# Performance work log

Measured on AMD Instinct MI355X. Metric: run time of the kernel, lower is better.

Reference implementation:

```python
import jax, jax.numpy as jnp
from jax import lax
import numpy as np

NPOINT = 1024
NSAMPLE = 32
BN_EPS = 1e-3  # Keras BatchNormalization default epsilon


def farthest_point_sample(xyz, npoint):
    # xyz: [B, N, 3] -> indices [B, npoint] (int32), sequential O(npoint*N)
    B, N, _ = xyz.shape

    def step(carry, _):
        distance, farthest = carry                                   # [B,N], [B]
        centroid = jnp.take_along_axis(xyz, farthest[:, None, None], axis=1)  # [B,1,3]
        dist = jnp.sum((xyz - centroid) ** 2, axis=-1)               # [B,N]
        distance = jnp.minimum(distance, dist)
        new_farthest = jnp.argmax(distance, axis=1).astype(jnp.int32)
        return (distance, new_farthest), farthest

    init = (jnp.full((B, N), 1e10, xyz.dtype), jnp.zeros((B,), jnp.int32))
    _, idxs = lax.scan(step, init, xs=None, length=npoint)           # [npoint, B]
    return jnp.transpose(idxs)                                       # [B, npoint]


def index_points_2d(points, idx):
    # points: [B,N,C], idx: [B,S] -> [B,S,C]
    return jnp.take_along_axis(points, idx[:, :, None], axis=1)


def index_points_3d(points, idx):
    # points: [B,N,C], idx: [B,S,K] -> [B,S,K,C]
    return jax.vmap(lambda p, i: p[i])(points, idx)


def query_ball_point(nsample, xyz, new_xyz):
    # nearest-nsample variant (radius is ignored, matching the source)
    # sq_dist: [B, S, N]
    sq = jnp.sum(new_xyz ** 2, axis=-1, keepdims=True) \
         - 2.0 * jnp.einsum('bsc,bnc->bsn', new_xyz, xyz) \
         + jnp.sum(xyz ** 2, axis=-1)[:, None, :]
    _, group_idx = lax.top_k(-sq, nsample)                           # [B,S,K]
    return group_idx


def bn_relu(x, g, b, mm, mv):
    # inference-mode BatchNorm (moving stats) + ReLU, per-channel on last dim
    return jax.nn.relu((x - mm) * lax.rsqrt(mv + BN_EPS) * g + b)


def setup_inputs() -> dict:
    key = jax.random.key(0)
    ks = jax.random.split(key, 20)
    B, N, D = 4, 16384, 64
    mlp = [64, 64, 128]
    cin = 3 + D  # 67
    inp = {
        'xyz': jax.random.normal(ks[0], (B, N, 3), jnp.float32),
        'points': jax.random.normal(ks[1], (B, N, D), jnp.float32),
    }
    c = cin
    for i, co in enumerate(mlp):
        inp[f'w{i}'] = jax.random.normal(ks[2 + 4 * i], (c, co), jnp.float32) * (1.0 / np.sqrt(c))
        inp[f'g{i}'] = jnp.ones((co,), jnp.float32)
        inp[f'b{i}'] = jnp.zeros((co,), jnp.float32)
        inp[f'mm{i}'] = jax.random.normal(ks[3 + 4 * i], (co,), jnp.float32) * 0.1
        inp[f'mv{i}'] = jax.random.uniform(ks[4 + 4 * i], (co,), jnp.float32, 0.5, 1.5)
        c = co
    return inp


def reference(xyz, points, w0, g0, b0, mm0, mv0, w1, g1, b1, mm1, mv1, w2, g2, b2, mm2, mv2):
    fps_idx = farthest_point_sample(xyz, NPOINT)                     # [B,S]
    new_xyz = index_points_2d(xyz, fps_idx)                          # [B,S,3]
    idx = query_ball_point(NSAMPLE, xyz, new_xyz)                    # [B,S,K]
    grouped_xyz = index_points_3d(xyz, idx)                          # [B,S,K,3]
    grouped_xyz_norm = grouped_xyz - new_xyz[:, :, None, :]
    grouped_points = index_points_3d(points, idx)                    # [B,S,K,D]
    x = jnp.concatenate([grouped_xyz_norm, grouped_points], axis=-1) # [B,S,K,3+D]
    for w, g, b, mm, mv in ((w0, g0, b0, mm0, mv0), (w1, g1, b1, mm1, mv1), (w2, g2, b2, mm2, mv2)):
        x = bn_relu(jnp.einsum('bskc,co->bsko', x, w), g, b, mm, mv)
    new_points = jnp.max(x, axis=2)                                  # [B,S,C_out]
    return (new_xyz, new_points)
```

## Files before the change

### kernel.cpp

```cpp
#include <hip/hip_runtime.h>
#include <hip/hip_bf16.h>
#include <stdint.h>

#define N_PTS 16384
#define S_OUT 1024


__global__ __launch_bounds__(1024) void fps_kernel(
    const float* __restrict__ xyz,
    float* __restrict__ out_newxyz)
{
  const int b    = blockIdx.x;
  const int tid  = threadIdx.x;
  const int lane = tid & 63;
  const int wid  = tid >> 6;
  const float* base = xyz + (size_t)b * N_PTS * 3;

  float px[16], py[16], pz[16], dist[16];
#pragma unroll
  for (int i = 0; i < 16; ++i) {
    int n = tid * 16 + i;
    px[i] = base[n * 3 + 0];
    py[i] = base[n * 3 + 1];
    pz[i] = base[n * 3 + 2];
    dist[i] = 1e10f;
  }

  __shared__ unsigned long long sred[2][16];

  float cx = base[0], cy = base[1], cz = base[2];

  for (int s = 0; s < S_OUT; ++s) {
    if (tid == 0) {
      size_t o = ((size_t)b * S_OUT + s) * 3;
      out_newxyz[o + 0] = cx;
      out_newxyz[o + 1] = cy;
      out_newxyz[o + 2] = cz;
    }
    if (s == S_OUT - 1) break;

    float best  = -1.0f;
    int   bestI = 0;
#pragma unroll
    for (int i = 0; i < 16; ++i) {
      float dx = __fsub_rn(px[i], cx);
      float dy = __fsub_rn(py[i], cy);
      float dz = __fsub_rn(pz[i], cz);
      float dd = __fadd_rn(__fadd_rn(__fmul_rn(dx, dx), __fmul_rn(dy, dy)),
                           __fmul_rn(dz, dz));
      float dm = fminf(dist[i], dd);
      dist[i] = dm;
      bool c = dm > best;
      best  = c ? dm : best;
      bestI = c ? i  : bestI;
    }
    const unsigned bestN = (unsigned)(tid * 16 + bestI);

    float m = best;
#pragma unroll
    for (int off = 1; off < 64; off <<= 1)
      m = fmaxf(m, __shfl_xor(m, off));
    unsigned long long msk = __ballot(best == m);
    int wl = __ffsll(msk) - 1;
    unsigned wn = (unsigned)__shfl((int)bestN, wl);

    const int p = s & 1;
    if (lane == 0)
      sred[p][wid] = ((unsigned long long)__float_as_uint(m) << 32) |
                     (unsigned long long)(0xFFFFFFFFu - wn);
    __syncthreads();

    unsigned long long k = sred[p][lane & 15];
#pragma unroll
    for (int off = 1; off < 16; off <<= 1) {
      unsigned long long o = __shfl_xor(k, off);
      if (o > k) k = o;
    }
    unsigned n = 0xFFFFFFFFu - (unsigned)(k & 0xFFFFFFFFull);
    n = __builtin_amdgcn_readfirstlane(n);
    const float* pc = base + (size_t)n * 3;
    cx = pc[0]; cy = pc[1]; cz = pc[2];
  }
}

__global__ __launch_bounds__(256, 2) void knn_kernel(
    const float* __restrict__ xyz,
    const float* __restrict__ newxyz,
    int* __restrict__ knn_out)
{
  const int bs  = blockIdx.x;
  const int b   = bs >> 10;
  const int tid = threadIdx.x;
  const float* base = xyz + (size_t)b * N_PTS * 3;

  const float qx = newxyz[(size_t)bs * 3 + 0];
  const float qy = newxyz[(size_t)bs * 3 + 1];
  const float qz = newxyz[(size_t)bs * 3 + 2];
  const float sumq = __fadd_rn(__fadd_rn(__fmul_rn(qx, qx), __fmul_rn(qy, qy)),
                               __fmul_rn(qz, qz));

  __shared__ unsigned hist[2048];
  __shared__ unsigned tsum[256];
  __shared__ unsigned long long cand[512];
  __shared__ unsigned long long s_min;
  __shared__ int s_b1, s_r1, s_b2, s_r2, s_cntL, s_cntC;

  for (int i = tid; i < 2048; i += 256) hist[i] = 0;
  if (tid == 0) { s_cntL = 0; s_cntC = 0; }
  __syncthreads();

#define KNN_KEY(n, u)                                                          \
    float x = base[(n) * 3 + 0];                                               \
    float y = base[(n) * 3 + 1];                                               \
    float z = base[(n) * 3 + 2];                                               \
    float sumx = __fadd_rn(__fadd_rn(__fmul_rn(x, x), __fmul_rn(y, y)),        \
                           __fmul_rn(z, z));                                   \
    float dot  = __fmul_rn(qx, x);                                             \
    dot = fmaf(qy, y, dot);                                                    \
    dot = fmaf(qz, z, dot);                                                    \
    float sq   = __fsub_rn(__fadd_rn(sumq, sumx), __fmul_rn(2.0f, dot));       \
    unsigned u = __float_as_uint(sq);                                          \
    u ^= (u & 0x80000000u) ? 0xFFFFFFFFu : 0x80000000u;

  for (int j = 0; j < 64; ++j) {
    int n = j * 256 + tid;
    KNN_KEY(n, u)
    atomicAdd(&hist[u >> 21], 1u);
  }
  __syncthreads();

  unsigned ts = 0;
#pragma unroll
  for (int u = 0; u < 8; ++u) ts += hist[tid * 8 + u];
  tsum[tid] = ts;
  __syncthreads();

  if (tid == 0) {
    unsigned acc = 0; int t2 = 0;
    for (; t2 < 256; ++t2) { unsigned h = tsum[t2]; if (acc + h >= 32u) break; acc += h; }
    int u2 = t2 * 8;
    for (;; ++u2) { unsigned h = hist[u2]; if (acc + h >= 32u) break; acc += h; }
    s_b1 = u2; s_r1 = 32 - (int)acc;
  }
  __syncthreads();
  const unsigned b1 = (unsigned)s_b1;
  const int r1 = s_r1;

  for (int i = tid; i < 2048; i += 256) hist[i] = 0;
  __syncthreads();

  for (int j = 0; j < 64; ++j) {
    int n = j * 256 + tid;
    KNN_KEY(n, u)
    if ((u >> 21) == b1) atomicAdd(&hist[(u >> 10) & 0x7FFu], 1u);
  }
  __syncthreads();

  ts = 0;
#pragma unroll
  for (int u = 0; u < 8; ++u) ts += hist[tid * 8 + u];
  tsum[tid] = ts;
  __syncthreads();

  if (tid == 0) {
    unsigned acc = 0; int t2 = 0;
    for (; t2 < 256; ++t2) { unsigned h = tsum[t2]; if (acc + h >= (unsigned)r1) break; acc += h; }
    int u2 = t2 * 8;
    for (;; ++u2) { unsigned h = hist[u2]; if (acc + h >= (unsigned)r1) break; acc += h; }
    s_b2 = u2; s_r2 = r1 - (int)acc;
  }
  __syncthreads();
  const unsigned b2 = (unsigned)s_b2;

  int* outp = knn_out + (size_t)bs * 32;

  for (int j = 0; j < 64; ++j) {
    int n = j * 256 + tid;
    KNN_KEY(n, u)
    unsigned bin = u >> 21;
    if (bin < b1) {
      int p = atomicAdd(&s_cntL, 1);
      outp[p] = n;
    } else if (bin == b1) {
      unsigned sub = (u >> 10) & 0x7FFu;
      if (sub < b2) {
        int p = atomicAdd(&s_cntL, 1);
        outp[p] = n;
      } else if (sub == b2) {
        int p = atomicAdd(&s_cntC, 1);
        if (p < 512) cand[p] = ((unsigned long long)u << 32) | (unsigned)n;
      }
    }
  }
  __syncthreads();
#undef KNN_KEY

  const int r   = s_r2;
  const int cl  = s_cntL;
  const int cnt = min(s_cntC, 512);
  unsigned long long last = 0ull;
  for (int i = 0; i < r; ++i) {
    if (tid == 0) s_min = ~0ull;
    __syncthreads();
    for (int p = tid; p < cnt; p += 256) {
      unsigned long long v = cand[p];
      if (i == 0 ? 1 : (v > last)) atomicMin(&s_min, v);
    }
    __syncthreads();
    unsigned long long m = s_min;
    if (tid == 0) outp[cl + i] = (int)(unsigned)(m & 0xFFFFFFFFull);
    last = m;
    __syncthreads();
  }
}

__global__ __launch_bounds__(256, 2) void mlp_kernel(
    const float* __restrict__ xyz,
    const float* __restrict__ points,
    const float* __restrict__ newxyz,
    const int* __restrict__ knn,
    const float* __restrict__ w0, const float* __restrict__ g0,
    const float* __restrict__ b0, const float* __restrict__ mm0,
    const float* __restrict__ mv0,
    const float* __restrict__ w1, const float* __restrict__ g1,
    const float* __restrict__ b1_, const float* __restrict__ mm1,
    const float* __restrict__ mv1,
    const float* __restrict__ w2, const float* __restrict__ g2,
    const float* __restrict__ b2_, const float* __restrict__ mm2,
    const float* __restrict__ mv2,
    float* __restrict__ out1)
{
  const int tid = threadIdx.x;
  const int BS0 = blockIdx.x * 2;

  __shared__ __align__(16) float xT[2][67][36];
  __shared__ __align__(16) float a1[2][64][36];
  __shared__ __align__(16) float wbuf[8192];

  {
    const int sg = tid >> 7;
    const int j  = (tid >> 2) & 31;
    const int cq = tid & 3;
    const int S  = BS0 + sg;
    const int bb = S >> 10;
    const int n  = knn[(size_t)S * 32 + j] & (N_PTS - 1);
    const float* pbase = points + ((size_t)bb * N_PTS + n) * 64;
    const float* xbase = xyz + ((size_t)bb * N_PTS + n) * 3;
    for (int c = cq; c < 67; c += 4) {
      float v;
      if (c < 3) v = __fsub_rn(xbase[c], newxyz[(size_t)S * 3 + c]);
      else       v = pbase[c - 3];
      xT[sg][c][j] = v;
    }
  }
  for (int i = tid; i < 67 * 64; i += 256) wbuf[i] = w0[i];
  __syncthreads();

  const int sg = tid >> 7;
  const int t  = tid & 127;

  {
    const int ot = t & 15, kt = t >> 4;
    const int o0 = ot * 4, k0 = kt * 4;
    float acc[4][4] = {};
    for (int c = 0; c < 67; ++c) {
      float4 xv = *(const float4*)&xT[sg][c][k0];
      float4 wq = *(const float4*)&wbuf[c * 64 + o0];
      float wv[4] = { wq.x, wq.y, wq.z, wq.w };
      float xs[4] = { xv.x, xv.y, xv.z, xv.w };
#pragma unroll
      for (int a = 0; a < 4; ++a)
#pragma unroll
        for (int k2 = 0; k2 < 4; ++k2)
          acc[a][k2] = fmaf(wv[a], xs[k2], acc[a][k2]);
    }
#pragma unroll
    for (int jj = 0; jj < 4; ++jj) {
      int o = o0 + jj;
      float A  = rsqrtf(mv0[o] + 1e-3f) * g0[o];
      float Bc = b0[o] - mm0[o] * A;
      float4 y;
      y.x = fmaxf(fmaf(acc[jj][0], A, Bc), 0.0f);
      y.y = fmaxf(fmaf(acc[jj][1], A, Bc), 0.0f);
      y.z = fmaxf(fmaf(acc[jj][2], A, Bc), 0.0f);
      y.w = fmaxf(fmaf(acc[jj][3], A, Bc), 0.0f);
      *(float4*)&a1[sg][o][k0] = y;
    }
  }
  __syncthreads();
  for (int i = tid; i < 64 * 64; i += 256) wbuf[i] = w1[i];
  __syncthreads();

  {
    const int ot = t & 15, kt = t >> 4;
    const int o0 = ot * 4, k0 = kt * 4;
    float acc[4][4] = {};
    for (int c = 0; c < 64; ++c) {
      float4 xv = *(const float4*)&a1[sg][c][k0];
      float4 wq = *(const float4*)&wbuf[c * 64 + o0];
      float wv[4] = { wq.x, wq.y, wq.z, wq.w };
      float xs[4] = { xv.x, xv.y, xv.z, xv.w };
#pragma unroll
      for (int a = 0; a < 4; ++a)
#pragma unroll
        for (int k2 = 0; k2 < 4; ++k2)
          acc[a][k2] = fmaf(wv[a], xs[k2], acc[a][k2]);
    }
#pragma unroll
    for (int jj = 0; jj < 4; ++jj) {
      int o = o0 + jj;
      float A  = rsqrtf(mv1[o] + 1e-3f) * g1[o];
      float Bc = b1_[o] - mm1[o] * A;
      float4 y;
      y.x = fmaxf(fmaf(acc[jj][0], A, Bc), 0.0f);
      y.y = fmaxf(fmaf(acc[jj][1], A, Bc), 0.0f);
      y.z = fmaxf(fmaf(acc[jj][2], A, Bc), 0.0f);
      y.w = fmaxf(fmaf(acc[jj][3], A, Bc), 0.0f);
      *(float4*)&xT[sg][o][k0] = y;
    }
  }
  __syncthreads();
  for (int i = tid; i < 64 * 128; i += 256) wbuf[i] = w2[i];
  __syncthreads();

  float* pm = &a1[0][0][0];
  {
    const int ot = t & 31, kt = t >> 5;
    const int o0 = ot * 4, k0 = kt * 8;
    float acc[4][8] = {};
    for (int c = 0; c < 64; ++c) {
      float4 xa = *(const float4*)&xT[sg][c][k0];
      float4 xb = *(const float4*)&xT[sg][c][k0 + 4];
      float4 wq = *(const float4*)&wbuf[c * 128 + o0];
      float wv[4] = { wq.x, wq.y, wq.z, wq.w };
      float xs[8] = { xa.x, xa.y, xa.z, xa.w, xb.x, xb.y, xb.z, xb.w };
#pragma unroll
      for (int a = 0; a < 4; ++a)
#pragma unroll
        for (int k2 = 0; k2 < 8; ++k2)
          acc[a][k2] = fmaf(wv[a], xs[k2], acc[a][k2]);
    }
#pragma unroll
    for (int jj = 0; jj < 4; ++jj) {
      int o = o0 + jj;
      float A  = rsqrtf(mv2[o] + 1e-3f) * g2[o];
      float Bc = b2_[o] - mm2[o] * A;
      float m = 0.0f;
#pragma unroll
      for (int kk = 0; kk < 8; ++kk)
        m = fmaxf(m, fmaf(acc[jj][kk], A, Bc));
      pm[((sg * 128 + o) << 2) + kt] = m;
    }
  }
  __syncthreads();
  {
    const int sg2 = tid >> 7, o = tid & 127;
    const int basep = (sg2 * 128 + o) << 2;
    float m = fmaxf(fmaxf(pm[basep + 0], pm[basep + 1]),
                    fmaxf(pm[basep + 2], pm[basep + 3]));
    out1[(size_t)(BS0 + sg2) * 128 + o] = m;
  }
}

extern "C" void kernel_launch(void* const* d_in, const int* in_sizes, int n_in,
                              void* d_out, int out_size, void* d_ws, size_t ws_size,
                              hipStream_t stream) {
  const float* xyz    = (const float*)d_in[0];
  const float* points = (const float*)d_in[1];
  const float* w0  = (const float*)d_in[2];
  const float* g0  = (const float*)d_in[3];
  const float* b0  = (const float*)d_in[4];
  const float* mm0 = (const float*)d_in[5];
  const float* mv0 = (const float*)d_in[6];
  const float* w1  = (const float*)d_in[7];
  const float* g1  = (const float*)d_in[8];
  const float* b1  = (const float*)d_in[9];
  const float* mm1 = (const float*)d_in[10];
  const float* mv1 = (const float*)d_in[11];
  const float* w2  = (const float*)d_in[12];
  const float* g2  = (const float*)d_in[13];
  const float* b2  = (const float*)d_in[14];
  const float* mm2 = (const float*)d_in[15];
  const float* mv2 = (const float*)d_in[16];

  float* out      = (float*)d_out;
  float* out_pts  = out + (size_t)4 * 1024 * 3;
  int*   knn      = (int*)d_ws;

  fps_kernel<<<4, 1024, 0, stream>>>(xyz, out);
  knn_kernel<<<4096, 256, 0, stream>>>(xyz, out, knn);
  mlp_kernel<<<2048, 256, 0, stream>>>(xyz, points, out, knn,
      w0, g0, b0, mm0, mv0, w1, g1, b1, mm1, mv1, w2, g2, b2, mm2, mv2,
      out_pts);
}
```

Before: 2.182 ms.

## Restructure FPS with packed float2 math, 512 threads, and two-phase argmax

Rewrites the farthest-point-sampling kernel to run 512 threads, each holding 32 points as packed float2 vectors, so distance updates can use packed FP32 instructions. The per-step argmax becomes a value-only max reduction across waves followed by an atomicMin on the index in shared memory, taken only by threads whose local max matches. This drops the 64-bit key packing and the index shuffles. It adds a second barrier per step and more registers per thread. Fixed lowest-index tie-breaking depends on the atomicMin and the reverse scan.

```diff
diff --git a/kernel.cpp b/kernel.cpp
--- a/kernel.cpp
+++ b/kernel.cpp
@@ -6,27 +6,35 @@
 #define S_OUT 1024
 
 
-__global__ __launch_bounds__(1024) void fps_kernel(
+typedef float v2f __attribute__((ext_vector_type(2)));
+
+__global__ __launch_bounds__(512)
+__attribute__((amdgpu_waves_per_eu(2, 2)))
+void fps_kernel(
     const float* __restrict__ xyz,
     float* __restrict__ out_newxyz)
 {
+#pragma clang fp contract(off)
   const int b    = blockIdx.x;
   const int tid  = threadIdx.x;
   const int lane = tid & 63;
   const int wid  = tid >> 6;
   const float* base = xyz + (size_t)b * N_PTS * 3;
 
-  float px[16], py[16], pz[16], dist[16];
+  v2f px[16], py[16], pz[16], dist[16];
 #pragma unroll
   for (int i = 0; i < 16; ++i) {
-    int n = tid * 16 + i;
-    px[i] = base[n * 3 + 0];
-    py[i] = base[n * 3 + 1];
-    pz[i] = base[n * 3 + 2];
-    dist[i] = 1e10f;
-  }
-
-  __shared__ unsigned long long sred[2][16];
+    int n0 = (tid * 32 + 2 * i) * 3;
+    px[i] = (v2f){ base[n0 + 0], base[n0 + 3] };
+    py[i] = (v2f){ base[n0 + 1], base[n0 + 4] };
+    pz[i] = (v2f){ base[n0 + 2], base[n0 + 5] };
+    dist[i] = (v2f){ 1e10f, 1e10f };
+  }
+
+  __shared__ float swave[2][8];
+  __shared__ unsigned s_idx[2];
+
+  if (tid == 0) { s_idx[0] = 0xFFFFFFFFu; s_idx[1] = 0xFFFFFFFFu; }
 
   float cx = base[0], cy = base[1], cz = base[2];
 
@@ -39,44 +47,55 @@
     }
     if (s == S_OUT - 1) break;
 
-    float best  = -1.0f;
-    int   bestI = 0;
+    const v2f cx2 = (v2f){ cx, cx };
+    const v2f cy2 = (v2f){ cy, cy };
+    const v2f cz2 = (v2f){ cz, cz };
+
+    float m0 = -1.0f, m1 = -1.0f, m2 = -1.0f, m3 = -1.0f;
 #pragma unroll
     for (int i = 0; i < 16; ++i) {
-      float dx = __fsub_rn(px[i], cx);
-      float dy = __fsub_rn(py[i], cy);
-      float dz = __fsub_rn(pz[i], cz);
-      float dd = __fadd_rn(__fadd_rn(__fmul_rn(dx, dx), __fmul_rn(dy, dy)),
-                           __fmul_rn(dz, dz));
-      float dm = fminf(dist[i], dd);
+      v2f dx = px[i] - cx2;
+      v2f dy = py[i] - cy2;
+      v2f dz = pz[i] - cz2;
+      v2f dd = (dx * dx + dy * dy) + dz * dz;
+      v2f dm = __builtin_elementwise_min(dist[i], dd);
       dist[i] = dm;
-      bool c = dm > best;
-      best  = c ? dm : best;
-      bestI = c ? i  : bestI;
-    }
-    const unsigned bestN = (unsigned)(tid * 16 + bestI);
-
-    float m = best;
+      if ((i & 3) == 0)      m0 = fmaxf(fmaxf(m0, dm.x), dm.y);
+      else if ((i & 3) == 1) m1 = fmaxf(fmaxf(m1, dm.x), dm.y);
+      else if ((i & 3) == 2) m2 = fmaxf(fmaxf(m2, dm.x), dm.y);
+      else                   m3 = fmaxf(fmaxf(m3, dm.x), dm.y);
+    }
+    const float lm = fmaxf(fmaxf(m0, m1), fmaxf(m2, m3));
+
+    float wm = lm;
 #pragma unroll
     for (int off = 1; off < 64; off <<= 1)
-      m = fmaxf(m, __shfl_xor(m, off));
-    unsigned long long msk = __ballot(best == m);
-    int wl = __ffsll(msk) - 1;
-    unsigned wn = (unsigned)__shfl((int)bestN, wl);
+      wm = fmaxf(wm, __shfl_xor(wm, off));
 
     const int p = s & 1;
-    if (lane == 0)
-      sred[p][wid] = ((unsigned long long)__float_as_uint(m) << 32) |
-                     (unsigned long long)(0xFFFFFFFFu - wn);
+    if (lane == 0) swave[p][wid] = wm;
     __syncthreads();
 
-    unsigned long long k = sred[p][lane & 15];
-#pragma unroll
-    for (int off = 1; off < 16; off <<= 1) {
-      unsigned long long o = __shfl_xor(k, off);
-      if (o > k) k = o;
-    }
-    unsigned n = 0xFFFFFFFFu - (unsigned)(k & 0xFFFFFFFFull);
+    float M = swave[p][0];
+    {
+      float a = fmaxf(fmaxf(swave[p][1], swave[p][2]), swave[p][3]);
+      float c = fmaxf(fmaxf(swave[p][4], swave[p][5]), swave[p][6]);
+      M = fmaxf(fmaxf(M, swave[p][7]), fmaxf(a, c));
+    }
+
+    if (lm == M) {
+      int bi = 0;
+#pragma unroll
+      for (int j = 31; j >= 0; --j) {
+        float d = dist[j >> 1][j & 1];
+        bi = (d == M) ? j : bi;
+      }
+      atomicMin(&s_idx[p], (unsigned)(tid * 32 + bi));
+    }
+    if (tid == 0) s_idx[p ^ 1] = 0xFFFFFFFFu;
+    __syncthreads();
+
+    unsigned n = s_idx[p];
     n = __builtin_amdgcn_readfirstlane(n);
     const float* pc = base + (size_t)n * 3;
     cx = pc[0]; cy = pc[1]; cz = pc[2];
@@ -387,7 +406,7 @@
   float* out_pts  = out + (size_t)4 * 1024 * 3;
   int*   knn      = (int*)d_ws;
 
-  fps_kernel<<<4, 1024, 0, stream>>>(xyz, out);
+  fps_kernel<<<4, 512, 0, stream>>>(xyz, out);
   knn_kernel<<<4096, 256, 0, stream>>>(xyz, out, knn);
   mlp_kernel<<<2048, 256, 0, stream>>>(xyz, points, out, knn,
       w0, g0, b0, mm0, mv0, w1, g1, b1, mm1, mv1, w2, g2, b2, mm2, mv2,
```

Measured after the change: 1.962 ms. 1.11x faster.
